# Optimization experiments

Hardware: AMD Instinct MI355X
Metric: run time of the kernel (lower is better)

## Reference

```python
import jax, jax.numpy as jnp
import numpy as np

NUM_CLASSES = 32
TRI = NUM_CLASSES * (NUM_CLASSES - 1) // 2      # 496 class pairs
HID = 32 * TRI                                  # 15872 total hidden
IN = 512
B = 256
RATIO = 0.0

# pair -> (i, j) class indices, in the same enumeration order as the torch idx formula
_I_IDX, _J_IDX = np.triu_indices(NUM_CLASSES, k=1)
_I_IDX = jnp.asarray(_I_IDX)
_J_IDX = jnp.asarray(_J_IDX)


def setup_inputs() -> dict:
    key = jax.random.key(0)
    ks = jax.random.split(key, 7)
    s = 0.02  # small init so activations stay sane
    return {
        "x": jax.random.normal(ks[0], (B, IN), jnp.float32),
        "W1": jax.random.normal(ks[1], (IN, HID), jnp.float32) * s,
        "b1": jax.random.normal(ks[2], (HID,), jnp.float32) * s,
        "W2": jax.random.normal(ks[3], (HID, HID), jnp.float32) * s,
        "b2": jax.random.normal(ks[4], (HID,), jnp.float32) * s,
        "Wout": jax.random.normal(ks[5], (HID, 2 * TRI), jnp.float32) * s,
        "bout": jax.random.normal(ks[6], (2 * TRI,), jnp.float32) * s,
    }


def reference(x, W1, b1, W2, b2, Wout, bout):
    # MLP stack: fc1 + relu, fc2 + relu (num_layers=2), fc_out
    h = jax.nn.relu(x @ W1 + b1)                 # [B, HID]
    h = jax.nn.relu(h @ W2 + b2)                 # [B, HID]
    out = h @ Wout + bout                        # [B, 2*TRI]

    # vote scatter: out[:, 2p], out[:, 2p+1] are the (i, j) logits of pair p
    pair = out.reshape(B, TRI, 2)                # [B, TRI, 2]
    d = pair[..., 0] - pair[..., 1]              # [B, TRI]
    # original condition: d > ratio  OR  -d >= ratio   (always true at ratio=0)
    mask = (d > RATIO) | (-d >= RATIO)
    vi = jnp.where(mask, pair[..., 0], 0.0)      # contribution to class i
    vj = jnp.where(mask, pair[..., 1], 0.0)      # contribution to class j

    votes = jnp.zeros((B, NUM_CLASSES), jnp.float32)
    votes = votes.at[:, _I_IDX].add(vi)
    votes = votes.at[:, _J_IDX].add(vj)
    return votes
```

## Files before the change

### kernel.cpp

```cpp
#include <hip/hip_runtime.h>
#include <hip/hip_bf16.h>

using short8 = __attribute__((ext_vector_type(8))) short;
using f32x16 = __attribute__((ext_vector_type(16))) float;
using us4    = __attribute__((ext_vector_type(4))) unsigned short;

#define NHID 15872

__device__ __forceinline__ unsigned short f2bf(float f) {
  unsigned u = __builtin_bit_cast(unsigned, f);
  u += 0x7fff + ((u >> 16) & 1);
  return (unsigned short)(u >> 16);
}
__device__ __forceinline__ short f2bf_hw(float f) {
  __hip_bfloat16 h = __float2bfloat16(f);
  return __builtin_bit_cast(short, h);
}
__device__ __forceinline__ float bf2f(unsigned short h) {
  return __builtin_bit_cast(float, ((unsigned)h) << 16);
}

__device__ __forceinline__ void gload16(const void* g, void* l) {
  __builtin_amdgcn_global_load_lds(
      (const __attribute__((address_space(1))) unsigned int*)g,
      (__attribute__((address_space(3))) unsigned int*)l, 16, 0, 0);
}
__device__ __forceinline__ void gload16nt(const void* g, void* l) {
  __builtin_amdgcn_global_load_lds(
      (const __attribute__((address_space(1))) unsigned int*)g,
      (__attribute__((address_space(3))) unsigned int*)l, 16, 0, 2);
}

__device__ __forceinline__ size_t pk_idx(int row, int col) {
  return (size_t)(col >> 4) * 4096 +
         (size_t)(row + 256 * ((col >> 3) & 1)) * 8 + (col & 7);
}

__global__ void cvt_x_pack(const float* __restrict__ x, unsigned short* __restrict__ xpk) {
  int g = blockIdx.x * 256 + threadIdx.x;
  int row = g >> 6, k0 = (g & 63) * 8;
  const float* p = x + (size_t)row * 512 + k0;
  float4 a = *reinterpret_cast<const float4*>(p);
  float4 b = *reinterpret_cast<const float4*>(p + 4);
  us4 o0, o1;
  o0[0] = f2bf(a.x); o0[1] = f2bf(a.y); o0[2] = f2bf(a.z); o0[3] = f2bf(a.w);
  o1[0] = f2bf(b.x); o1[1] = f2bf(b.y); o1[2] = f2bf(b.z); o1[3] = f2bf(b.w);
  unsigned short* d = xpk + pk_idx(row, k0);
  *reinterpret_cast<us4*>(d)     = o0;
  *reinterpret_cast<us4*>(d + 4) = o1;
}


#define WAITV(N) asm volatile("s_waitcnt vmcnt(" #N ")" ::: "memory")

#define STAGEB(BUF, T) do { \
    gload16nt(bsrc + (size_t)(T) * 32 * NHID,       &Blds[BUF][(w * 4 + 0) * 128]); \
    gload16nt(bsrc + ((size_t)(T) * 32 + 2) * NHID, &Blds[BUF][(w * 4 + 2) * 128]); \
  } while (0)

#define LOADA(T) do { \
    const unsigned short* ap_ = asrc + (size_t)(T) * 8192; \
    rA[0] = *reinterpret_cast<const short8*>(ap_); \
    rA[1] = *reinterpret_cast<const short8*>(ap_ + 4096); \
    rA[2] = *reinterpret_cast<const short8*>(ap_ + 256); \
    rA[3] = *reinterpret_cast<const short8*>(ap_ + 4096 + 256); \
  } while (0)

#define COMPUTE(BC) do { \
    const float* bb_ = &Blds[BC][0]; \
    _Pragma("unroll") \
    for (int ks_ = 0; ks_ < 2; ++ks_) { \
      short8 bfr_[2]; \
      _Pragma("unroll") \
      for (int nb_ = 0; nb_ < 2; ++nb_) { \
        float tf_[8]; \
        _Pragma("unroll") \
        for (int jj_ = 0; jj_ < 8; ++jj_) \
          tf_[jj_] = bb_[(ks_ * 16 + hi * 8 + jj_) * 128 + wn * 64 + nb_ * 32 + l31]; \
        _Pragma("unroll") \
        for (int jj_ = 0; jj_ < 8; ++jj_) bfr_[nb_][jj_] = f2bf_hw(tf_[jj_]); \
      } \
      acc[0] = __builtin_amdgcn_mfma_f32_32x32x16_bf16(rA[ks_],     bfr_[0], acc[0], 0, 0, 0); \
      acc[1] = __builtin_amdgcn_mfma_f32_32x32x16_bf16(rA[ks_],     bfr_[1], acc[1], 0, 0, 0); \
      acc[2] = __builtin_amdgcn_mfma_f32_32x32x16_bf16(rA[2 + ks_], bfr_[0], acc[2], 0, 0, 0); \
      acc[3] = __builtin_amdgcn_mfma_f32_32x32x16_bf16(rA[2 + ks_], bfr_[1], acc[3], 0, 0, 0); \
    } \
  } while (0)

template<int OUTMODE, bool SWZ>
__global__ __launch_bounds__(512, 4)
void gemm_v15(const unsigned short* __restrict__ Apk, int KC,
              const float* __restrict__ B, const float* __restrict__ bias,
              unsigned short* __restrict__ Cf, unsigned short* __restrict__ Cpb)
{
  __shared__ float Blds[3][32 * 128];

  int nidx, ks0;
  if (SWZ) {
    int b = blockIdx.x;
    ks0  = b & 7;
    nidx = b >> 3;
  } else {
    nidx = blockIdx.x; ks0 = blockIdx.y;
  }
  const int n0   = nidx * 128;
  const int k0   = ks0 * KC;
  const int tid  = threadIdx.x;
  const int w    = tid >> 6;
  const int lane = tid & 63;
  const int l31  = lane & 31;
  const int hi   = lane >> 5;
  const int wm   = w >> 1;
  const int wn   = w & 1;

  f32x16 acc[4] = {};
  short8 rA[4];

  const float* bsrc = B + (size_t)(k0 + w * 4 + hi) * NHID + n0 + l31 * 4;
  const unsigned short* asrc = Apk + (size_t)(k0 >> 4) * 4096 +
                               (size_t)(wm * 64 + l31 + 256 * hi) * 8;

  const int NT = KC >> 5;

  STAGEB(0, 0);
  STAGEB(1, 1);

  int bc = 0;
  for (int t = 0; t < NT; ++t) {
    if (t + 1 < NT) { WAITV(2); } else { WAITV(0); }
    __builtin_amdgcn_sched_barrier(0);
    __builtin_amdgcn_s_barrier();
    LOADA(t);
    if (t + 2 < NT) { int sb_ = bc >= 1 ? bc - 1 : 2; STAGEB(sb_, t + 2); }
    COMPUTE(bc);
    bc = bc == 2 ? 0 : bc + 1;
  }

#pragma unroll
  for (int rb = 0; rb < 2; ++rb) {
#pragma unroll
    for (int nb = 0; nb < 2; ++nb) {
      int col = n0 + wn * 64 + nb * 32 + l31;
      float bv = (OUTMODE != 1) ? bias[col] : 0.f;
#pragma unroll
      for (int reg = 0; reg < 16; ++reg) {
        int row = wm * 64 + rb * 32 + (reg & 3) + 8 * (reg >> 2) + 4 * hi;
        float v = acc[rb * 2 + nb][reg];
        if (OUTMODE == 0) {
          v += bv; v = v > 0.f ? v : 0.f;
          Cf[pk_idx(row, col)] = f2bf(v);
        } else if (OUTMODE == 1) {
          Cpb[(size_t)ks0 * 256 * NHID + (size_t)row * NHID + col] = f2bf(v);
        } else {
          v += bv; v = v > 0.f ? v : 0.f;
          Cf[(size_t)row * NHID + col] = f2bf(v);
        }
      }
    }
  }
}

template<bool PACK>
__global__ void reduce_hb(const unsigned short* __restrict__ part,
                          const float* __restrict__ bias,
                          unsigned short* __restrict__ out, int S) {
  int g8 = blockIdx.x * 256 + threadIdx.x;
  int row = g8 / 1984;
  int c   = (g8 - row * 1984) * 8;
  size_t off = (size_t)row * NHID + c;
  float s[8] = {0.f, 0.f, 0.f, 0.f, 0.f, 0.f, 0.f, 0.f};
  for (int k = 0; k < S; ++k) {
    short8 p = *reinterpret_cast<const short8*>(part + (size_t)k * 256 * NHID + off);
#pragma unroll
    for (int j = 0; j < 8; ++j) s[j] += bf2f((unsigned short)p[j]);
  }
  short8 o;
#pragma unroll
  for (int j = 0; j < 8; ++j) {
    float v = s[j] + bias[c + j];
    v = v > 0.f ? v : 0.f;
    o[j] = (short)f2bf(v);
  }
  if (PACK) *reinterpret_cast<short8*>(out + pk_idx(row, c)) = o;
  else      *reinterpret_cast<short8*>(out + off) = o;
}

__global__ void wv_fold(const float* __restrict__ Wout, float* __restrict__ Wv) {
  int g = blockIdx.x * 256 + threadIdx.x;
  int k = g >> 5, c = g & 31;
  const float* row = Wout + (size_t)k * 992;
  float s = 0.f;
#pragma unroll
  for (int o = 0; o < 32; ++o) {
    if (o == c) continue;
    int i = c < o ? c : o;
    int j = c < o ? o : c;
    int p = 31 * i - (i * (i - 1)) / 2 + (j - i - 1);
    s += row[2 * p + (c > o ? 1 : 0)];
  }
  Wv[g] = s;
}

__global__ void votes_partial(const unsigned short* __restrict__ h2,
                              const float* __restrict__ Wv,
                              float* __restrict__ part) {
  int bm = blockIdx.x >> 5;
  int ks = blockIdx.x & 31;
  int r  = bm * 8 + (threadIdx.x >> 5);
  int c  = threadIdx.x & 31;
  const unsigned short* hrow = h2 + (size_t)r * NHID + ks * 496;
  const float* wp = Wv + (size_t)(ks * 496) * 32 + c;
  float s = 0.f;
  for (int k0 = 0; k0 < 496; k0 += 8) {
    short8 hv = *reinterpret_cast<const short8*>(hrow + k0);
#pragma unroll
    for (int j = 0; j < 8; ++j)
      s += bf2f((unsigned short)hv[j]) * wp[(size_t)(k0 + j) * 32];
  }
  part[(size_t)(ks * 256 + r) * 32 + c] = s;
}

__global__ void votes_reduce(const float* __restrict__ part,
                             const float* __restrict__ bout,
                             float* __restrict__ out) {
  int g = blockIdx.x * 256 + threadIdx.x;
  int c = g & 31;
  float s = 0.f;
#pragma unroll
  for (int ks = 0; ks < 32; ++ks) s += part[(size_t)ks * 8192 + g];
  float bv = 0.f;
#pragma unroll
  for (int o = 0; o < 32; ++o) {
    if (o == c) continue;
    int i = c < o ? c : o;
    int j = c < o ? o : c;
    int p = 31 * i - (i * (i - 1)) / 2 + (j - i - 1);
    bv += bout[2 * p + (c > o ? 1 : 0)];
  }
  out[g] = s + bv;
}

extern "C" void kernel_launch(void* const* d_in, const int* in_sizes, int n_in,
                              void* d_out, int out_size, void* d_ws, size_t ws_size,
                              hipStream_t stream) {
  const float* x    = (const float*)d_in[0];
  const float* W1   = (const float*)d_in[1];
  const float* b1   = (const float*)d_in[2];
  const float* W2   = (const float*)d_in[3];
  const float* b2   = (const float*)d_in[4];
  const float* Wout = (const float*)d_in[5];
  const float* bout = (const float*)d_in[6];
  float* out = (float*)d_out;

  char* ws = (char*)d_ws;
  unsigned short* xpk  = (unsigned short*)(ws);
  unsigned short* h1pk = (unsigned short*)(ws + 262144);
  unsigned short* h2   = (unsigned short*)(ws + 8388608);
  float*          Wv   = (float*)(ws + 16515072);
  float*          part = (float*)(ws + 18546688);
  unsigned short* pb   = (unsigned short*)(ws + 19595264);

  const size_t PARTB = (size_t)256 * NHID * 2;
  const bool split = ws_size >= 19595264ull + 8 * PARTB;

  hipLaunchKernelGGL(cvt_x_pack, dim3(64), dim3(256), 0, stream, x, xpk);
  if (split) {
    hipLaunchKernelGGL((gemm_v15<1, false>), dim3(124, 2), dim3(512), 0, stream,
                       xpk, 256, W1, (const float*)nullptr,
                       (unsigned short*)nullptr, pb);
    hipLaunchKernelGGL((reduce_hb<true>), dim3(1984), dim3(256), 0, stream,
                       pb, b1, h1pk, 2);
    hipLaunchKernelGGL((gemm_v15<1, true>), dim3(992), dim3(512), 0, stream,
                       h1pk, 1984, W2, (const float*)nullptr,
                       (unsigned short*)nullptr, pb);
    hipLaunchKernelGGL((reduce_hb<false>), dim3(1984), dim3(256), 0, stream,
                       pb, b2, h2, 8);
  } else {
    hipLaunchKernelGGL((gemm_v15<0, false>), dim3(124, 1), dim3(512), 0, stream,
                       xpk, 512, W1, b1, h1pk, (unsigned short*)nullptr);
    hipLaunchKernelGGL((gemm_v15<2, false>), dim3(124, 1), dim3(512), 0, stream,
                       h1pk, NHID, W2, b2, h2, (unsigned short*)nullptr);
  }
  hipLaunchKernelGGL(wv_fold,       dim3(1984), dim3(256), 0, stream, Wout, Wv);
  hipLaunchKernelGGL(votes_partial, dim3(1024), dim3(256), 0, stream, h2, Wv, part);
  hipLaunchKernelGGL(votes_reduce,  dim3(32),   dim3(256), 0, stream, part, bout, out);
}
```

Before: 393.0 us.

## Retile GEMM to 64x512 blocks with double-buffered 16-row K stages

```diff
diff --git a/kernel.cpp b/kernel.cpp
--- a/kernel.cpp
+++ b/kernel.cpp
@@ -24,11 +24,6 @@
   __builtin_amdgcn_global_load_lds(
       (const __attribute__((address_space(1))) unsigned int*)g,
       (__attribute__((address_space(3))) unsigned int*)l, 16, 0, 0);
-}
-__device__ __forceinline__ void gload16nt(const void* g, void* l) {
-  __builtin_amdgcn_global_load_lds(
-      (const __attribute__((address_space(1))) unsigned int*)g,
-      (__attribute__((address_space(3))) unsigned int*)l, 16, 0, 2);
 }
 
 __device__ __forceinline__ size_t pk_idx(int row, int col) {
@@ -54,97 +49,89 @@
 #define WAITV(N) asm volatile("s_waitcnt vmcnt(" #N ")" ::: "memory")
 
 #define STAGEB(BUF, T) do { \
-    gload16nt(bsrc + (size_t)(T) * 32 * NHID,       &Blds[BUF][(w * 4 + 0) * 128]); \
-    gload16nt(bsrc + ((size_t)(T) * 32 + 2) * NHID, &Blds[BUF][(w * 4 + 2) * 128]); \
+    const float* bp_ = bsrc + (size_t)((T) * 16 + 2 * w) * NHID; \
+    gload16(bp_,              &Blds[BUF][(2 * w) * 512]); \
+    gload16(bp_ + 256,        &Blds[BUF][(2 * w) * 512 + 256]); \
+    gload16(bp_ + NHID,       &Blds[BUF][(2 * w + 1) * 512]); \
+    gload16(bp_ + NHID + 256, &Blds[BUF][(2 * w + 1) * 512 + 256]); \
   } while (0)
 
 #define LOADA(T) do { \
-    const unsigned short* ap_ = asrc + (size_t)(T) * 8192; \
+    const unsigned short* ap_ = asrc + (size_t)(T) * 4096; \
     rA[0] = *reinterpret_cast<const short8*>(ap_); \
-    rA[1] = *reinterpret_cast<const short8*>(ap_ + 4096); \
-    rA[2] = *reinterpret_cast<const short8*>(ap_ + 256); \
-    rA[3] = *reinterpret_cast<const short8*>(ap_ + 4096 + 256); \
+    rA[1] = *reinterpret_cast<const short8*>(ap_ + 256); \
   } while (0)
 
-#define COMPUTE(BC) do { \
-    const float* bb_ = &Blds[BC][0]; \
+#define COMPUTE(BUF) do { \
+    const float* bb_ = &Blds[BUF][0]; \
     _Pragma("unroll") \
-    for (int ks_ = 0; ks_ < 2; ++ks_) { \
-      short8 bfr_[2]; \
+    for (int nb_ = 0; nb_ < 2; ++nb_) { \
+      float tf_[8]; \
       _Pragma("unroll") \
-      for (int nb_ = 0; nb_ < 2; ++nb_) { \
-        float tf_[8]; \
-        _Pragma("unroll") \
-        for (int jj_ = 0; jj_ < 8; ++jj_) \
-          tf_[jj_] = bb_[(ks_ * 16 + hi * 8 + jj_) * 128 + wn * 64 + nb_ * 32 + l31]; \
-        _Pragma("unroll") \
-        for (int jj_ = 0; jj_ < 8; ++jj_) bfr_[nb_][jj_] = f2bf_hw(tf_[jj_]); \
-      } \
-      acc[0] = __builtin_amdgcn_mfma_f32_32x32x16_bf16(rA[ks_],     bfr_[0], acc[0], 0, 0, 0); \
-      acc[1] = __builtin_amdgcn_mfma_f32_32x32x16_bf16(rA[ks_],     bfr_[1], acc[1], 0, 0, 0); \
-      acc[2] = __builtin_amdgcn_mfma_f32_32x32x16_bf16(rA[2 + ks_], bfr_[0], acc[2], 0, 0, 0); \
-      acc[3] = __builtin_amdgcn_mfma_f32_32x32x16_bf16(rA[2 + ks_], bfr_[1], acc[3], 0, 0, 0); \
+      for (int jj_ = 0; jj_ < 8; ++jj_) \
+        tf_[jj_] = bb_[(hi * 8 + jj_) * 512 + w * 64 + nb_ * 32 + l31]; \
+      short8 bfr_; \
+      _Pragma("unroll") \
+      for (int jj_ = 0; jj_ < 8; ++jj_) bfr_[jj_] = f2bf_hw(tf_[jj_]); \
+      acc[nb_]     = __builtin_amdgcn_mfma_f32_32x32x16_bf16(rA[0], bfr_, acc[nb_],     0, 0, 0); \
+      acc[2 + nb_] = __builtin_amdgcn_mfma_f32_32x32x16_bf16(rA[1], bfr_, acc[2 + nb_], 0, 0, 0); \
     } \
   } while (0)
 
 template<int OUTMODE, bool SWZ>
 __global__ __launch_bounds__(512, 4)
-void gemm_v15(const unsigned short* __restrict__ Apk, int KC,
+void gemm_v16(const unsigned short* __restrict__ Apk, int KC,
               const float* __restrict__ B, const float* __restrict__ bias,
               unsigned short* __restrict__ Cf, unsigned short* __restrict__ Cpb)
 {
-  __shared__ float Blds[3][32 * 128];
-
-  int nidx, ks0;
+  __shared__ float Blds[2][16 * 512];
+
+  int m0, nidx, ks0;
   if (SWZ) {
     int b = blockIdx.x;
-    ks0  = b & 7;
-    nidx = b >> 3;
+    int low3 = b & 7, m = (b >> 3) & 3, high = b >> 5;
+    int nk = high * 8 + low3;
+    if (nk >= 124) return;
+    ks0 = nk & 3; nidx = nk >> 2; m0 = m * 64;
   } else {
-    nidx = blockIdx.x; ks0 = blockIdx.y;
-  }
-  const int n0   = nidx * 128;
+    m0 = blockIdx.x * 64; nidx = blockIdx.y; ks0 = blockIdx.z;
+  }
+  const int n0   = nidx * 512;
   const int k0   = ks0 * KC;
   const int tid  = threadIdx.x;
   const int w    = tid >> 6;
   const int lane = tid & 63;
   const int l31  = lane & 31;
   const int hi   = lane >> 5;
-  const int wm   = w >> 1;
-  const int wn   = w & 1;
 
   f32x16 acc[4] = {};
-  short8 rA[4];
-
-  const float* bsrc = B + (size_t)(k0 + w * 4 + hi) * NHID + n0 + l31 * 4;
+  short8 rA[2];
+
+  const float* bsrc = B + (size_t)k0 * NHID + n0 + lane * 4;
   const unsigned short* asrc = Apk + (size_t)(k0 >> 4) * 4096 +
-                               (size_t)(wm * 64 + l31 + 256 * hi) * 8;
-
-  const int NT = KC >> 5;
+                               (size_t)(m0 + l31 + 256 * hi) * 8;
+
+  const int NT = KC >> 4;
 
   STAGEB(0, 0);
-  STAGEB(1, 1);
-
-  int bc = 0;
   for (int t = 0; t < NT; ++t) {
-    if (t + 1 < NT) { WAITV(2); } else { WAITV(0); }
+    WAITV(0);
     __builtin_amdgcn_sched_barrier(0);
     __builtin_amdgcn_s_barrier();
     LOADA(t);
-    if (t + 2 < NT) { int sb_ = bc >= 1 ? bc - 1 : 2; STAGEB(sb_, t + 2); }
-    COMPUTE(bc);
-    bc = bc == 2 ? 0 : bc + 1;
+    if (t + 1 < NT) STAGEB((t + 1) & 1, t + 1);
+    COMPUTE(t & 1);
   }
 
 #pragma unroll
   for (int rb = 0; rb < 2; ++rb) {
 #pragma unroll
     for (int nb = 0; nb < 2; ++nb) {
-      int col = n0 + wn * 64 + nb * 32 + l31;
+      int col = n0 + w * 64 + nb * 32 + l31;
       float bv = (OUTMODE != 1) ? bias[col] : 0.f;
 #pragma unroll
       for (int reg = 0; reg < 16; ++reg) {
-        int row = wm * 64 + rb * 32 + (reg & 3) + 8 * (reg >> 2) + 4 * hi;
+        int row = m0 + rb * 32 + (reg & 3) + 8 * (reg >> 2) + 4 * hi;
         float v = acc[rb * 2 + nb][reg];
         if (OUTMODE == 0) {
           v += bv; v = v > 0.f ? v : 0.f;
@@ -261,24 +248,21 @@
   unsigned short* pb   = (unsigned short*)(ws + 19595264);
 
   const size_t PARTB = (size_t)256 * NHID * 2;
-  const bool split = ws_size >= 19595264ull + 8 * PARTB;
+  const bool split = ws_size >= 19595264ull + 4 * PARTB;
 
   hipLaunchKernelGGL(cvt_x_pack, dim3(64), dim3(256), 0, stream, x, xpk);
   if (split) {
-    hipLaunchKernelGGL((gemm_v15<1, false>), dim3(124, 2), dim3(512), 0, stream,
-                       xpk, 256, W1, (const float*)nullptr,
-                       (unsigned short*)nullptr, pb);
-    hipLaunchKernelGGL((reduce_hb<true>), dim3(1984), dim3(256), 0, stream,
-                       pb, b1, h1pk, 2);
-    hipLaunchKernelGGL((gemm_v15<1, true>), dim3(992), dim3(512), 0, stream,
-                       h1pk, 1984, W2, (const float*)nullptr,
+    hipLaunchKernelGGL((gemm_v16<0, false>), dim3(4, 31, 1), dim3(512), 0, stream,
+                       xpk, 512, W1, b1, h1pk, (unsigned short*)nullptr);
+    hipLaunchKernelGGL((gemm_v16<1, true>), dim3(512), dim3(512), 0, stream,
+                       h1pk, 3968, W2, (const float*)nullptr,
                        (unsigned short*)nullptr, pb);
     hipLaunchKernelGGL((reduce_hb<false>), dim3(1984), dim3(256), 0, stream,
-                       pb, b2, h2, 8);
+                       pb, b2, h2, 4);
   } else {
-    hipLaunchKernelGGL((gemm_v15<0, false>), dim3(124, 1), dim3(512), 0, stream,
+    hipLaunchKernelGGL((gemm_v16<0, false>), dim3(4, 31, 1), dim3(512), 0, stream,
                        xpk, 512, W1, b1, h1pk, (unsigned short*)nullptr);
-    hipLaunchKernelGGL((gemm_v15<2, false>), dim3(124, 1), dim3(512), 0, stream,
+    hipLaunchKernelGGL((gemm_v16<2, false>), dim3(4, 31, 1), dim3(512), 0, stream,
                        h1pk, NHID, W2, b2, h2, (unsigned short*)nullptr);
   }
   hipLaunchKernelGGL(wv_fold,       dim3(1984), dim3(256), 0, stream, Wout, Wv);
```

Result: slower. 524.9 us (+33.6%).

## Halve W2 split-K, fuse second reduction into vote projection, drop NT loads

Applied to the files above, without the earlier changes.

```diff
diff --git a/kernel.cpp b/kernel.cpp
--- a/kernel.cpp
+++ b/kernel.cpp
@@ -6,6 +6,7 @@
 using us4    = __attribute__((ext_vector_type(4))) unsigned short;
 
 #define NHID 15872
+#define PLANE ((size_t)256 * NHID)
 
 __device__ __forceinline__ unsigned short f2bf(float f) {
   unsigned u = __builtin_bit_cast(unsigned, f);
@@ -24,11 +25,6 @@
   __builtin_amdgcn_global_load_lds(
       (const __attribute__((address_space(1))) unsigned int*)g,
       (__attribute__((address_space(3))) unsigned int*)l, 16, 0, 0);
-}
-__device__ __forceinline__ void gload16nt(const void* g, void* l) {
-  __builtin_amdgcn_global_load_lds(
-      (const __attribute__((address_space(1))) unsigned int*)g,
-      (__attribute__((address_space(3))) unsigned int*)l, 16, 0, 2);
 }
 
 __device__ __forceinline__ size_t pk_idx(int row, int col) {
@@ -54,8 +50,8 @@
 #define WAITV(N) asm volatile("s_waitcnt vmcnt(" #N ")" ::: "memory")
 
 #define STAGEB(BUF, T) do { \
-    gload16nt(bsrc + (size_t)(T) * 32 * NHID,       &Blds[BUF][(w * 4 + 0) * 128]); \
-    gload16nt(bsrc + ((size_t)(T) * 32 + 2) * NHID, &Blds[BUF][(w * 4 + 2) * 128]); \
+    gload16(bsrc + (size_t)(T) * 32 * NHID,       &Blds[BUF][(w * 4 + 0) * 128]); \
+    gload16(bsrc + ((size_t)(T) * 32 + 2) * NHID, &Blds[BUF][(w * 4 + 2) * 128]); \
   } while (0)
 
 #define LOADA(T) do { \
@@ -89,17 +85,18 @@
 
 template<int OUTMODE, bool SWZ>
 __global__ __launch_bounds__(512, 4)
-void gemm_v15(const unsigned short* __restrict__ Apk, int KC,
-              const float* __restrict__ B, const float* __restrict__ bias,
-              unsigned short* __restrict__ Cf, unsigned short* __restrict__ Cpb)
+void gemm_k2(const unsigned short* __restrict__ Apk, int KC,
+             const float* __restrict__ B, const float* __restrict__ bias,
+             unsigned short* __restrict__ Cf, unsigned short* __restrict__ Cpb)
 {
   __shared__ float Blds[3][32 * 128];
 
   int nidx, ks0;
   if (SWZ) {
     int b = blockIdx.x;
-    ks0  = b & 7;
-    nidx = b >> 3;
+    int xcd = b & 7;
+    ks0  = xcd >> 1;
+    nidx = (b >> 3) * 2 + (xcd & 1);
   } else {
     nidx = blockIdx.x; ks0 = blockIdx.y;
   }
@@ -150,7 +147,7 @@
           v += bv; v = v > 0.f ? v : 0.f;
           Cf[pk_idx(row, col)] = f2bf(v);
         } else if (OUTMODE == 1) {
-          Cpb[(size_t)ks0 * 256 * NHID + (size_t)row * NHID + col] = f2bf(v);
+          Cpb[(size_t)ks0 * PLANE + (size_t)row * NHID + col] = f2bf(v);
         } else {
           v += bv; v = v > 0.f ? v : 0.f;
           Cf[(size_t)row * NHID + col] = f2bf(v);
@@ -160,17 +157,16 @@
   }
 }
 
-template<bool PACK>
-__global__ void reduce_hb(const unsigned short* __restrict__ part,
-                          const float* __restrict__ bias,
-                          unsigned short* __restrict__ out, int S) {
+__global__ void reduce_hb_pack(const unsigned short* __restrict__ part,
+                               const float* __restrict__ bias,
+                               unsigned short* __restrict__ out, int S) {
   int g8 = blockIdx.x * 256 + threadIdx.x;
   int row = g8 / 1984;
   int c   = (g8 - row * 1984) * 8;
   size_t off = (size_t)row * NHID + c;
   float s[8] = {0.f, 0.f, 0.f, 0.f, 0.f, 0.f, 0.f, 0.f};
   for (int k = 0; k < S; ++k) {
-    short8 p = *reinterpret_cast<const short8*>(part + (size_t)k * 256 * NHID + off);
+    short8 p = *reinterpret_cast<const short8*>(part + (size_t)k * PLANE + off);
 #pragma unroll
     for (int j = 0; j < 8; ++j) s[j] += bf2f((unsigned short)p[j]);
   }
@@ -181,8 +177,7 @@
     v = v > 0.f ? v : 0.f;
     o[j] = (short)f2bf(v);
   }
-  if (PACK) *reinterpret_cast<short8*>(out + pk_idx(row, c)) = o;
-  else      *reinterpret_cast<short8*>(out + off) = o;
+  *reinterpret_cast<short8*>(out + pk_idx(row, c)) = o;
 }
 
 __global__ void wv_fold(const float* __restrict__ Wout, float* __restrict__ Wv) {
@@ -199,6 +194,35 @@
     s += row[2 * p + (c > o ? 1 : 0)];
   }
   Wv[g] = s;
+}
+
+__global__ void votes_partial_f(const unsigned short* __restrict__ pb,
+                                const float* __restrict__ b2,
+                                const float* __restrict__ Wv,
+                                float* __restrict__ part) {
+  int bm = blockIdx.x >> 5;
+  int ks = blockIdx.x & 31;
+  int r  = bm * 8 + (threadIdx.x >> 5);
+  int c  = threadIdx.x & 31;
+  size_t rowoff = (size_t)r * NHID + ks * 496;
+  const float* wp = Wv + (size_t)(ks * 496) * 32 + c;
+  const float* bp = b2 + ks * 496;
+  float s = 0.f;
+  for (int k0 = 0; k0 < 496; k0 += 8) {
+    short8 p0 = *reinterpret_cast<const short8*>(pb + 0 * PLANE + rowoff + k0);
+    short8 p1 = *reinterpret_cast<const short8*>(pb + 1 * PLANE + rowoff + k0);
+    short8 p2 = *reinterpret_cast<const short8*>(pb + 2 * PLANE + rowoff + k0);
+    short8 p3 = *reinterpret_cast<const short8*>(pb + 3 * PLANE + rowoff + k0);
+#pragma unroll
+    for (int j = 0; j < 8; ++j) {
+      float h = bf2f((unsigned short)p0[j]) + bf2f((unsigned short)p1[j]) +
+                bf2f((unsigned short)p2[j]) + bf2f((unsigned short)p3[j]) +
+                bp[k0 + j];
+      h = h > 0.f ? h : 0.f;
+      s += h * wp[(size_t)(k0 + j) * 32];
+    }
+  }
+  part[(size_t)(ks * 256 + r) * 32 + c] = s;
 }
 
 __global__ void votes_partial(const unsigned short* __restrict__ h2,
@@ -260,28 +284,29 @@
   float*          part = (float*)(ws + 18546688);
   unsigned short* pb   = (unsigned short*)(ws + 19595264);
 
-  const size_t PARTB = (size_t)256 * NHID * 2;
-  const bool split = ws_size >= 19595264ull + 8 * PARTB;
+  const size_t PARTB = PLANE * 2;
+  const bool split = ws_size >= 19595264ull + 4 * PARTB;
 
   hipLaunchKernelGGL(cvt_x_pack, dim3(64), dim3(256), 0, stream, x, xpk);
   if (split) {
-    hipLaunchKernelGGL((gemm_v15<1, false>), dim3(124, 2), dim3(512), 0, stream,
+    hipLaunchKernelGGL((gemm_k2<1, false>), dim3(124, 2), dim3(512), 0, stream,
                        xpk, 256, W1, (const float*)nullptr,
                        (unsigned short*)nullptr, pb);
-    hipLaunchKernelGGL((reduce_hb<true>), dim3(1984), dim3(256), 0, stream,
+    hipLaunchKernelGGL(reduce_hb_pack, dim3(1984), dim3(256), 0, stream,
                        pb, b1, h1pk, 2);
-    hipLaunchKernelGGL((gemm_v15<1, true>), dim3(992), dim3(512), 0, stream,
-                       h1pk, 1984, W2, (const float*)nullptr,
+    hipLaunchKernelGGL((gemm_k2<1, true>), dim3(496), dim3(512), 0, stream,
+                       h1pk, 3968, W2, (const float*)nullptr,
                        (unsigned short*)nullptr, pb);
-    hipLaunchKernelGGL((reduce_hb<false>), dim3(1984), dim3(256), 0, stream,
-                       pb, b2, h2, 8);
+    hipLaunchKernelGGL(wv_fold, dim3(1984), dim3(256), 0, stream, Wout, Wv);
+    hipLaunchKernelGGL(votes_partial_f, dim3(1024), dim3(256), 0, stream,
+                       pb, b2, Wv, part);
   } else {
-    hipLaunchKernelGGL((gemm_v15<0, false>), dim3(124, 1), dim3(512), 0, stream,
+    hipLaunchKernelGGL((gemm_k2<0, false>), dim3(124, 1), dim3(512), 0, stream,
                        xpk, 512, W1, b1, h1pk, (unsigned short*)nullptr);
-    hipLaunchKernelGGL((gemm_v15<2, false>), dim3(124, 1), dim3(512), 0, stream,
+    hipLaunchKernelGGL((gemm_k2<2, false>), dim3(124, 1), dim3(512), 0, stream,
                        h1pk, NHID, W2, b2, h2, (unsigned short*)nullptr);
-  }
-  hipLaunchKernelGGL(wv_fold,       dim3(1984), dim3(256), 0, stream, Wout, Wv);
-  hipLaunchKernelGGL(votes_partial, dim3(1024), dim3(256), 0, stream, h2, Wv, part);
-  hipLaunchKernelGGL(votes_reduce,  dim3(32),   dim3(256), 0, stream, part, bout, out);
-}
+    hipLaunchKernelGGL(wv_fold, dim3(1984), dim3(256), 0, stream, Wout, Wv);
+    hipLaunchKernelGGL(votes_partial, dim3(1024), dim3(256), 0, stream, h2, Wv, part);
+  }
+  hipLaunchKernelGGL(votes_reduce, dim3(32), dim3(256), 0, stream, part, bout, out);
+}
```

New measurement: 394.5 us. About the same (+0.4%).
